# Optimization experiments

Hardware: AMD Instinct MI355X
Metric: run time of the kernel (lower is better)

## Reference

```python
import jax, jax.numpy as jnp
import numpy as np

EPS = 1e-5
G = 8    # groups
K = 3    # kernel_size


def bn(x, gamma, beta, mean, var):
    # inference-mode BatchNorm2d; x: (b,C,H,W), params: (C,)
    inv = gamma / jnp.sqrt(var + EPS)
    return x * inv[None, :, None, None] + (beta - mean * inv)[None, :, None, None]


def gconv1x1(x, w):
    # grouped 1x1 conv; x: (b, g*ci, H, W), w: (g, co, ci) -> (b, g*co, H, W)
    b, C, H, W = x.shape
    g, co, ci = w.shape
    xg = x.reshape(b, g, ci, H, W)
    y = jnp.einsum('bgihw,goi->bgohw', xg, w)
    return y.reshape(b, g * co, H, W)


def unfold3(x):
    # torch.nn.Unfold(k=3, stride=1, dilation=1, padding=1), reshaped to (b, C, 9, H, W)
    b, C, H, W = x.shape
    xp = jnp.pad(x, ((0, 0), (0, 0), (1, 1), (1, 1)))
    patches = [xp[:, :, i:i + H, j:j + W] for i in range(K) for j in range(K)]
    return jnp.stack(patches, axis=2)


def setup_inputs() -> dict:
    key = jax.random.key(0)
    ks = jax.random.split(key, 16)
    f = jax.random.normal
    u = jax.random.uniform
    return {
        'x':  f(ks[0], (2, 256, 128, 128), jnp.float32),
        'w1': f(ks[1], (8, 8, 32), jnp.float32) * 0.1,
        'b1': f(ks[2], (64,), jnp.float32) * 0.1,
        'g1': u(ks[3], (64,), jnp.float32, 0.5, 1.5),
        'be1': f(ks[4], (64,), jnp.float32) * 0.1,
        'm1': f(ks[5], (64,), jnp.float32) * 0.1,
        'v1': u(ks[6], (64,), jnp.float32, 0.5, 1.5),
        'w2': f(ks[7], (8, 10, 8), jnp.float32) * 0.1,
        'b2': f(ks[8], (80,), jnp.float32) * 0.1,
        'g2': u(ks[9], (80,), jnp.float32, 0.5, 1.5),
        'be2': f(ks[10], (80,), jnp.float32) * 0.1,
        'm2': f(ks[11], (80,), jnp.float32) * 0.1,
        'v2': u(ks[12], (80,), jnp.float32, 0.5, 1.5),
        'wv': f(ks[13], (8, 32, 32), jnp.float32) * 0.1,
    }


def reference(x, w1, b1, g1, be1, m1, v1, w2, b2, g2, be2, m2, v2, wv):
    b, C, H, W = x.shape
    # mask_conv: grouped 1x1 conv -> BN -> tanh -> grouped 1x1 conv -> BN
    t = jnp.tanh(bn(gconv1x1(x, w1) + b1[None, :, None, None], g1, be1, m1, v1))
    mn = bn(gconv1x1(t, w2) + b2[None, :, None, None], g2, be2, m2, v2)  # (b, G*(1+K*K), H, W)
    neighbor = mn[:, :G]          # (b, G, H, W)
    mask = mn[:, G:]              # (b, G*K*K, H, W)
    nb = unfold3(neighbor)        # (b, G, 9, H, W)
    logits = mask.reshape(b, G, K * K, H, W) + nb
    attn = jax.nn.softmax(logits, axis=2)               # (b, G, 9, H, W)
    # value path: grouped 1x1 conv (no bias) then unfold
    v = gconv1x1(x, wv)                                  # (b, C, H, W)
    vu = unfold3(v).reshape(b, G, C // G, K * K, H, W)   # (b, G, C/G, 9, H, W)
    out = jnp.einsum('bgkhw,bgckhw->bgchw', attn, vu)    # weighted sum over window
    return out.reshape(b, C, H, W)
```

## Files before the change

### kernel.cpp

```cpp
#include <hip/hip_runtime.h>
#include <hip/hip_bf16.h>

#define HW  16384
#define WD  128

#define TS   16
#define HS   18
#define HP   (HS * HS)
#define PRS  20
#define PLS  360

__device__ __forceinline__ unsigned short f2bf(float f) {
    unsigned int u = __builtin_bit_cast(unsigned int, f);
    u += 0x7FFFu + ((u >> 16) & 1u);
    return (unsigned short)(u >> 16);
}
__device__ __forceinline__ float bf2f(unsigned int s) {
    return __builtin_bit_cast(float, (s & 0xFFFFu) << 16);
}
__device__ __forceinline__ float ftanh(float v) {
    const float e = __expf(2.0f * v);
    return 1.0f - __fdividef(2.0f, e + 1.0f);
}

__global__ __launch_bounds__(256) void la_t(
    const float* __restrict__ x,
    const float* __restrict__ w1, const float* __restrict__ b1,
    const float* __restrict__ g1, const float* __restrict__ be1,
    const float* __restrict__ m1, const float* __restrict__ v1,
    const float* __restrict__ w2, const float* __restrict__ b2,
    const float* __restrict__ g2, const float* __restrict__ be2,
    const float* __restrict__ m2, const float* __restrict__ v2,
    unsigned short* __restrict__ t, float* __restrict__ nb)
{
    const int pix = blockIdx.x * blockDim.x + threadIdx.x;
    const int b   = blockIdx.y;
    const int p   = blockIdx.z;

    const float* xp = x + (size_t)(b * 256 + p * 32) * HW + pix;
    float xv[32];
#pragma unroll
    for (int c = 0; c < 32; ++c) xv[c] = xp[(size_t)c * HW];

    const float* w1p = w1 + p * 256;
    float tv[8];
#pragma unroll
    for (int o = 0; o < 8; ++o) {
        float a = 0.f;
#pragma unroll
        for (int ci = 0; ci < 32; ++ci) a = fmaf(xv[ci], w1p[o * 32 + ci], a);
        const int ch = p * 8 + o;
        const float inv = g1[ch] * rsqrtf(v1[ch] + 1e-5f);
        const float add = be1[ch] + (b1[ch] - m1[ch]) * inv;
        tv[o] = ftanh(fmaf(a, inv, add));
    }

    uint4 u;
    u.x = (unsigned)f2bf(tv[0]) | ((unsigned)f2bf(tv[1]) << 16);
    u.y = (unsigned)f2bf(tv[2]) | ((unsigned)f2bf(tv[3]) << 16);
    u.z = (unsigned)f2bf(tv[4]) | ((unsigned)f2bf(tv[5]) << 16);
    u.w = (unsigned)f2bf(tv[6]) | ((unsigned)f2bf(tv[7]) << 16);
    *(uint4*)(t + ((size_t)(b * 8 + p) * HW + pix) * 8) = u;

    if (p == 0) {
#pragma unroll
        for (int o = 0; o < 8; ++o) {
            float a = 0.f;
#pragma unroll
            for (int i = 0; i < 8; ++i) a = fmaf(tv[i], w2[o * 8 + i], a);
            const float inv = g2[o] * rsqrtf(v2[o] + 1e-5f);
            const float add = be2[o] + (b2[o] - m2[o]) * inv;
            nb[(size_t)(b * 8 + o) * HW + pix] = fmaf(a, inv, add);
        }
    }
}

__global__ __launch_bounds__(256, 4) void la_fused(
    const float* __restrict__ x,
    const float* __restrict__ w2, const float* __restrict__ b2,
    const float* __restrict__ g2, const float* __restrict__ be2,
    const float* __restrict__ m2, const float* __restrict__ v2,
    const float* __restrict__ wv,
    const unsigned short* __restrict__ t, const float* __restrict__ nb,
    float* __restrict__ out)
{
    __shared__ ushort4 xt[8 * PLS];
    __shared__ float   nbs[PLS];

    const int tid  = threadIdx.x;
    const int bg   = blockIdx.x;
    const int tile = blockIdx.y;
    const int b    = bg >> 3, g = bg & 7;
    const int ty0  = (tile >> 3) * TS;
    const int tx0  = (tile & 7) * TS;

    const float* xg  = x  + (size_t)(b * 256 + g * 32) * HW;
    const float* nbp = nb + (size_t)(b * 8 + g) * HW;

    for (int hp = tid; hp < HP; hp += 256) {
        const int hy = hp / HS, hx = hp - hy * HS;
        const int iy = ty0 + hy - 1, ix = tx0 + hx - 1;
        const int slot = hy * PRS + hx;
        if (((unsigned)iy < 128u) && ((unsigned)ix < 128u)) {
            const int po = iy * WD + ix;
            float xv[32];
#pragma unroll
            for (int c = 0; c < 32; ++c) xv[c] = xg[(size_t)c * HW + po];
            nbs[slot] = nbp[po];
#pragma unroll
            for (int c4 = 0; c4 < 8; ++c4)
                xt[c4 * PLS + slot] = make_ushort4(
                    f2bf(xv[c4 * 4 + 0]), f2bf(xv[c4 * 4 + 1]),
                    f2bf(xv[c4 * 4 + 2]), f2bf(xv[c4 * 4 + 3]));
        } else {
            const ushort4 z = make_ushort4(0, 0, 0, 0);
#pragma unroll
            for (int c4 = 0; c4 < 8; ++c4) xt[c4 * PLS + slot] = z;
            nbs[slot] = 0.f;
        }
    }
    __syncthreads();

    const int cy  = tid >> 4, cx = tid & 15;
    const int iy  = ty0 + cy, ix = tx0 + cx;
    const int pix = iy * WD + ix;

    const int mc0    = 8 + 9 * g;
    const int pa     = mc0 / 10;
    const int pb     = (mc0 + 8) / 10;
    const int ksplit = 10 - (mc0 - pa * 10);

    float tA[8], tB[8];
    {
        const uint4 ua = *(const uint4*)(t + ((size_t)(b * 8 + pa) * HW + pix) * 8);
        tA[0] = bf2f(ua.x); tA[1] = bf2f(ua.x >> 16);
        tA[2] = bf2f(ua.y); tA[3] = bf2f(ua.y >> 16);
        tA[4] = bf2f(ua.z); tA[5] = bf2f(ua.z >> 16);
        tA[6] = bf2f(ua.w); tA[7] = bf2f(ua.w >> 16);
    }
    if (pb != pa) {
        const uint4 ub = *(const uint4*)(t + ((size_t)(b * 8 + pb) * HW + pix) * 8);
        tB[0] = bf2f(ub.x); tB[1] = bf2f(ub.x >> 16);
        tB[2] = bf2f(ub.y); tB[3] = bf2f(ub.y >> 16);
        tB[4] = bf2f(ub.z); tB[5] = bf2f(ub.z >> 16);
        tB[6] = bf2f(ub.w); tB[7] = bf2f(ub.w >> 16);
    } else {
#pragma unroll
        for (int o = 0; o < 8; ++o) tB[o] = tA[o];
    }

    float lg[9];
    float mx = -1e30f;
#pragma unroll
    for (int k = 0; k < 9; ++k) {
        const int mc = mc0 + k;
        const int p  = (k < ksplit) ? pa : pb;
        const int o  = mc - p * 10;
        const float* w2p = w2 + p * 80 + o * 8;
        float a = 0.f;
#pragma unroll
        for (int i = 0; i < 8; ++i) {
            const float ti = (k < ksplit) ? tA[i] : tB[i];
            a = fmaf(ti, w2p[i], a);
        }
        const float inv = g2[mc] * rsqrtf(v2[mc] + 1e-5f);
        const float add = be2[mc] + (b2[mc] - m2[mc]) * inv;
        lg[k] = fmaf(a, inv, add) + nbs[(cy + k / 3) * PRS + (cx + k % 3)];
        mx = fmaxf(mx, lg[k]);
    }
    float ssum = 0.f;
#pragma unroll
    for (int k = 0; k < 9; ++k) { lg[k] = __expf(lg[k] - mx); ssum += lg[k]; }
    const float rs = 1.f / ssum;

    float s[32];
#pragma unroll
    for (int c = 0; c < 32; ++c) s[c] = 0.f;
#pragma unroll
    for (int k = 0; k < 9; ++k) {
        const int slot = (cy + k / 3) * PRS + (cx + k % 3);
        const float e = lg[k];
#pragma unroll
        for (int c4 = 0; c4 < 8; ++c4) {
            const ushort4 xv4 = xt[c4 * PLS + slot];
            s[c4 * 4 + 0] = fmaf(e, bf2f(xv4.x), s[c4 * 4 + 0]);
            s[c4 * 4 + 1] = fmaf(e, bf2f(xv4.y), s[c4 * 4 + 1]);
            s[c4 * 4 + 2] = fmaf(e, bf2f(xv4.z), s[c4 * 4 + 2]);
            s[c4 * 4 + 3] = fmaf(e, bf2f(xv4.w), s[c4 * 4 + 3]);
        }
    }

    const float* wvg = wv + g * 1024;
    float* og = out + (size_t)(b * 256 + g * 32) * HW + pix;
#pragma unroll 4
    for (int o = 0; o < 32; ++o) {
        const float* wp = wvg + o * 32;
        float a = 0.f;
#pragma unroll
        for (int ci = 0; ci < 32; ++ci) a = fmaf(s[ci], wp[ci], a);
        __builtin_nontemporal_store(a * rs, og + (size_t)o * HW);
    }
}

extern "C" void kernel_launch(void* const* d_in, const int* in_sizes, int n_in,
                              void* d_out, int out_size, void* d_ws, size_t ws_size,
                              hipStream_t stream)
{
    const float* x   = (const float*)d_in[0];
    const float* w1  = (const float*)d_in[1];
    const float* b1  = (const float*)d_in[2];
    const float* g1  = (const float*)d_in[3];
    const float* be1 = (const float*)d_in[4];
    const float* m1  = (const float*)d_in[5];
    const float* v1  = (const float*)d_in[6];
    const float* w2  = (const float*)d_in[7];
    const float* b2  = (const float*)d_in[8];
    const float* g2  = (const float*)d_in[9];
    const float* be2 = (const float*)d_in[10];
    const float* m2  = (const float*)d_in[11];
    const float* v2  = (const float*)d_in[12];
    const float* wv  = (const float*)d_in[13];

    float* out = (float*)d_out;
    unsigned short* t = (unsigned short*)d_ws;
    float* nb = (float*)(t + (size_t)2 * 8 * HW * 8);

    dim3 blk(256);
    dim3 gt(HW / 256, 2, 8);
    dim3 grd(16, 64);

    hipLaunchKernelGGL(la_t, gt, blk, 0, stream,
                       x, w1, b1, g1, be1, m1, v1, w2, b2, g2, be2, m2, v2,
                       t, nb);
    hipLaunchKernelGGL(la_fused, grd, blk, 0, stream,
                       x, w2, b2, g2, be2, m2, v2, wv, t, nb, out);
}
```

Baseline: 130.0 us.

## Fuse mask-conv stage into attention kernel, recomputing tanh features per tile

Merges the two launches into one kernel. Each block now recomputes the first grouped conv, BN and tanh for its own group over the halo tile and keeps the result in LDS. It also recomputes the neighbor logits from partition 0 per halo pixel, and the adjacent partition's features per center pixel. This removes the workspace round-trip for t/nb and one kernel launch. In exchange it adds redundant reads of x (partition 0 and the neighboring partition) and repeated conv1 compute, plus extra LDS use that may lower occupancy.

```diff
diff --git a/kernel.cpp b/kernel.cpp
--- a/kernel.cpp
+++ b/kernel.cpp
@@ -1,5 +1,4 @@
 #include <hip/hip_runtime.h>
-#include <hip/hip_bf16.h>
 
 #define HW  16384
 #define WD  128
@@ -23,7 +22,27 @@
     return 1.0f - __fdividef(2.0f, e + 1.0f);
 }
 
-__global__ __launch_bounds__(256) void la_t(
+__device__ __forceinline__ void conv1_bn_tanh(
+    const float xv[32], int p,
+    const float* __restrict__ w1, const float* __restrict__ g1,
+    const float* __restrict__ be1, const float* __restrict__ b1,
+    const float* __restrict__ m1, const float* __restrict__ v1,
+    float t[8])
+{
+    const float* w1g = w1 + p * 256;
+#pragma unroll
+    for (int o = 0; o < 8; ++o) {
+        float a = 0.f;
+#pragma unroll
+        for (int ci = 0; ci < 32; ++ci) a = fmaf(xv[ci], w1g[o * 32 + ci], a);
+        const int ch = p * 8 + o;
+        const float inv = g1[ch] * rsqrtf(v1[ch] + 1e-5f);
+        const float add = be1[ch] + (b1[ch] - m1[ch]) * inv;
+        t[o] = ftanh(fmaf(a, inv, add));
+    }
+}
+
+__global__ __launch_bounds__(256, 4) void la_all(
     const float* __restrict__ x,
     const float* __restrict__ w1, const float* __restrict__ b1,
     const float* __restrict__ g1, const float* __restrict__ be1,
@@ -31,60 +50,11 @@
     const float* __restrict__ w2, const float* __restrict__ b2,
     const float* __restrict__ g2, const float* __restrict__ be2,
     const float* __restrict__ m2, const float* __restrict__ v2,
-    unsigned short* __restrict__ t, float* __restrict__ nb)
-{
-    const int pix = blockIdx.x * blockDim.x + threadIdx.x;
-    const int b   = blockIdx.y;
-    const int p   = blockIdx.z;
-
-    const float* xp = x + (size_t)(b * 256 + p * 32) * HW + pix;
-    float xv[32];
-#pragma unroll
-    for (int c = 0; c < 32; ++c) xv[c] = xp[(size_t)c * HW];
-
-    const float* w1p = w1 + p * 256;
-    float tv[8];
-#pragma unroll
-    for (int o = 0; o < 8; ++o) {
-        float a = 0.f;
-#pragma unroll
-        for (int ci = 0; ci < 32; ++ci) a = fmaf(xv[ci], w1p[o * 32 + ci], a);
-        const int ch = p * 8 + o;
-        const float inv = g1[ch] * rsqrtf(v1[ch] + 1e-5f);
-        const float add = be1[ch] + (b1[ch] - m1[ch]) * inv;
-        tv[o] = ftanh(fmaf(a, inv, add));
-    }
-
-    uint4 u;
-    u.x = (unsigned)f2bf(tv[0]) | ((unsigned)f2bf(tv[1]) << 16);
-    u.y = (unsigned)f2bf(tv[2]) | ((unsigned)f2bf(tv[3]) << 16);
-    u.z = (unsigned)f2bf(tv[4]) | ((unsigned)f2bf(tv[5]) << 16);
-    u.w = (unsigned)f2bf(tv[6]) | ((unsigned)f2bf(tv[7]) << 16);
-    *(uint4*)(t + ((size_t)(b * 8 + p) * HW + pix) * 8) = u;
-
-    if (p == 0) {
-#pragma unroll
-        for (int o = 0; o < 8; ++o) {
-            float a = 0.f;
-#pragma unroll
-            for (int i = 0; i < 8; ++i) a = fmaf(tv[i], w2[o * 8 + i], a);
-            const float inv = g2[o] * rsqrtf(v2[o] + 1e-5f);
-            const float add = be2[o] + (b2[o] - m2[o]) * inv;
-            nb[(size_t)(b * 8 + o) * HW + pix] = fmaf(a, inv, add);
-        }
-    }
-}
-
-__global__ __launch_bounds__(256, 4) void la_fused(
-    const float* __restrict__ x,
-    const float* __restrict__ w2, const float* __restrict__ b2,
-    const float* __restrict__ g2, const float* __restrict__ be2,
-    const float* __restrict__ m2, const float* __restrict__ v2,
     const float* __restrict__ wv,
-    const unsigned short* __restrict__ t, const float* __restrict__ nb,
     float* __restrict__ out)
 {
     __shared__ ushort4 xt[8 * PLS];
+    __shared__ uint4   tls[PLS];
     __shared__ float   nbs[PLS];
 
     const int tid  = threadIdx.x;
@@ -94,8 +64,11 @@
     const int ty0  = (tile >> 3) * TS;
     const int tx0  = (tile & 7) * TS;
 
-    const float* xg  = x  + (size_t)(b * 256 + g * 32) * HW;
-    const float* nbp = nb + (size_t)(b * 8 + g) * HW;
+    const float* xb = x + (size_t)b * 256 * HW;
+    const float* xg = xb + (size_t)(g * 32) * HW;
+
+    const float inv2n = g2[g] * rsqrtf(v2[g] + 1e-5f);
+    const float add2n = be2[g] + (b2[g] - m2[g]) * inv2n;
 
     for (int hp = tid; hp < HP; hp += 256) {
         const int hy = hp / HS, hx = hp - hy * HS;
@@ -103,19 +76,46 @@
         const int slot = hy * PRS + hx;
         if (((unsigned)iy < 128u) && ((unsigned)ix < 128u)) {
             const int po = iy * WD + ix;
-            float xv[32];
-#pragma unroll
-            for (int c = 0; c < 32; ++c) xv[c] = xg[(size_t)c * HW + po];
-            nbs[slot] = nbp[po];
+            float xv[32], tg[8];
+            if (g == 0) {
+#pragma unroll
+                for (int c = 0; c < 32; ++c) xv[c] = xb[(size_t)c * HW + po];
+                conv1_bn_tanh(xv, 0, w1, g1, be1, b1, m1, v1, tg);
+                float an = 0.f;
+#pragma unroll
+                for (int i = 0; i < 8; ++i) an = fmaf(tg[i], w2[g * 8 + i], an);
+                nbs[slot] = fmaf(an, inv2n, add2n);
+            } else {
+                {
+                    float x0[32], t0[8];
+#pragma unroll
+                    for (int c = 0; c < 32; ++c) x0[c] = xb[(size_t)c * HW + po];
+                    conv1_bn_tanh(x0, 0, w1, g1, be1, b1, m1, v1, t0);
+                    float an = 0.f;
+#pragma unroll
+                    for (int i = 0; i < 8; ++i) an = fmaf(t0[i], w2[g * 8 + i], an);
+                    nbs[slot] = fmaf(an, inv2n, add2n);
+                }
+#pragma unroll
+                for (int c = 0; c < 32; ++c) xv[c] = xg[(size_t)c * HW + po];
+                conv1_bn_tanh(xv, g, w1, g1, be1, b1, m1, v1, tg);
+            }
 #pragma unroll
             for (int c4 = 0; c4 < 8; ++c4)
                 xt[c4 * PLS + slot] = make_ushort4(
                     f2bf(xv[c4 * 4 + 0]), f2bf(xv[c4 * 4 + 1]),
                     f2bf(xv[c4 * 4 + 2]), f2bf(xv[c4 * 4 + 3]));
+            uint4 tu;
+            tu.x = (unsigned)f2bf(tg[0]) | ((unsigned)f2bf(tg[1]) << 16);
+            tu.y = (unsigned)f2bf(tg[2]) | ((unsigned)f2bf(tg[3]) << 16);
+            tu.z = (unsigned)f2bf(tg[4]) | ((unsigned)f2bf(tg[5]) << 16);
+            tu.w = (unsigned)f2bf(tg[6]) | ((unsigned)f2bf(tg[7]) << 16);
+            tls[slot] = tu;
         } else {
             const ushort4 z = make_ushort4(0, 0, 0, 0);
 #pragma unroll
             for (int c4 = 0; c4 < 8; ++c4) xt[c4 * PLS + slot] = z;
+            tls[slot] = make_uint4(0u, 0u, 0u, 0u);
             nbs[slot] = 0.f;
         }
     }
@@ -132,18 +132,18 @@
 
     float tA[8], tB[8];
     {
-        const uint4 ua = *(const uint4*)(t + ((size_t)(b * 8 + pa) * HW + pix) * 8);
+        const uint4 ua = tls[(cy + 1) * PRS + (cx + 1)];
         tA[0] = bf2f(ua.x); tA[1] = bf2f(ua.x >> 16);
         tA[2] = bf2f(ua.y); tA[3] = bf2f(ua.y >> 16);
         tA[4] = bf2f(ua.z); tA[5] = bf2f(ua.z >> 16);
         tA[6] = bf2f(ua.w); tA[7] = bf2f(ua.w >> 16);
     }
     if (pb != pa) {
-        const uint4 ub = *(const uint4*)(t + ((size_t)(b * 8 + pb) * HW + pix) * 8);
-        tB[0] = bf2f(ub.x); tB[1] = bf2f(ub.x >> 16);
-        tB[2] = bf2f(ub.y); tB[3] = bf2f(ub.y >> 16);
-        tB[4] = bf2f(ub.z); tB[5] = bf2f(ub.z >> 16);
-        tB[6] = bf2f(ub.w); tB[7] = bf2f(ub.w >> 16);
+        float xv[32];
+        const float* xn = xb + (size_t)(pb * 32) * HW + pix;
+#pragma unroll
+        for (int c = 0; c < 32; ++c) xv[c] = xn[(size_t)c * HW];
+        conv1_bn_tanh(xv, pb, w1, g1, be1, b1, m1, v1, tB);
     } else {
 #pragma unroll
         for (int o = 0; o < 8; ++o) tB[o] = tA[o];
@@ -222,16 +222,12 @@
     const float* wv  = (const float*)d_in[13];
 
     float* out = (float*)d_out;
-    unsigned short* t = (unsigned short*)d_ws;
-    float* nb = (float*)(t + (size_t)2 * 8 * HW * 8);
+    (void)d_ws; (void)ws_size;
 
     dim3 blk(256);
-    dim3 gt(HW / 256, 2, 8);
     dim3 grd(16, 64);
 
-    hipLaunchKernelGGL(la_t, gt, blk, 0, stream,
+    hipLaunchKernelGGL(la_all, grd, blk, 0, stream,
                        x, w1, b1, g1, be1, m1, v1, w2, b2, g2, be2, m2, v2,
-                       t, nb);
-    hipLaunchKernelGGL(la_fused, grd, blk, 0, stream,
-                       x, w2, b2, g2, be2, m2, v2, wv, t, nb, out);
-}
+                       wv, out);
+}
```

Result: slower. 137.2 us (+5.6%).

## Move value projection and full mask conv into pre-pass kernel

Applied to the files above, without the earlier changes.

The first kernel now computes the value 1x1 grouped conv (stored as bf16) plus the full second mask conv (neighbor and mask logits) per pixel. The attention kernel then only gathers the bf16 value halo and the precomputed logits and writes the weighted sum directly. This removes the per-pixel 32x32 projection after aggregation and the t round-trip, but the pre-pass does more work and writes more intermediate data (bf16 v, plus the 72-channel mask in fp32). Because the projection now runs before the window sum, it is rounded to bf16 and reapplied to neighbor values, which changes the precision profile.

```diff
diff --git a/kernel.cpp b/kernel.cpp
--- a/kernel.cpp
+++ b/kernel.cpp
@@ -1,5 +1,4 @@
 #include <hip/hip_runtime.h>
-#include <hip/hip_bf16.h>
 
 #define HW  16384
 #define WD  128
@@ -23,7 +22,7 @@
     return 1.0f - __fdividef(2.0f, e + 1.0f);
 }
 
-__global__ __launch_bounds__(256) void la_t(
+__global__ __launch_bounds__(256) void la_pre(
     const float* __restrict__ x,
     const float* __restrict__ w1, const float* __restrict__ b1,
     const float* __restrict__ g1, const float* __restrict__ be1,
@@ -31,7 +30,8 @@
     const float* __restrict__ w2, const float* __restrict__ b2,
     const float* __restrict__ g2, const float* __restrict__ be2,
     const float* __restrict__ m2, const float* __restrict__ v2,
-    unsigned short* __restrict__ t, float* __restrict__ nb)
+    const float* __restrict__ wv,
+    uint4* __restrict__ v4, float* __restrict__ nb, float* __restrict__ mask)
 {
     const int pix = blockIdx.x * blockDim.x + threadIdx.x;
     const int b   = blockIdx.y;
@@ -42,49 +42,62 @@
 #pragma unroll
     for (int c = 0; c < 32; ++c) xv[c] = xp[(size_t)c * HW];
 
-    const float* w1p = w1 + p * 256;
+    const float* w1g = w1 + p * 256;
     float tv[8];
 #pragma unroll
     for (int o = 0; o < 8; ++o) {
         float a = 0.f;
 #pragma unroll
-        for (int ci = 0; ci < 32; ++ci) a = fmaf(xv[ci], w1p[o * 32 + ci], a);
+        for (int ci = 0; ci < 32; ++ci) a = fmaf(xv[ci], w1g[o * 32 + ci], a);
         const int ch = p * 8 + o;
         const float inv = g1[ch] * rsqrtf(v1[ch] + 1e-5f);
         const float add = be1[ch] + (b1[ch] - m1[ch]) * inv;
         tv[o] = ftanh(fmaf(a, inv, add));
     }
 
-    uint4 u;
-    u.x = (unsigned)f2bf(tv[0]) | ((unsigned)f2bf(tv[1]) << 16);
-    u.y = (unsigned)f2bf(tv[2]) | ((unsigned)f2bf(tv[3]) << 16);
-    u.z = (unsigned)f2bf(tv[4]) | ((unsigned)f2bf(tv[5]) << 16);
-    u.w = (unsigned)f2bf(tv[6]) | ((unsigned)f2bf(tv[7]) << 16);
-    *(uint4*)(t + ((size_t)(b * 8 + p) * HW + pix) * 8) = u;
-
-    if (p == 0) {
-#pragma unroll
-        for (int o = 0; o < 8; ++o) {
+#pragma unroll
+    for (int o = 0; o < 10; ++o) {
+        const int c = p * 10 + o;
+        float a = 0.f;
+#pragma unroll
+        for (int i = 0; i < 8; ++i) a = fmaf(tv[i], w2[p * 80 + o * 8 + i], a);
+        const float inv = g2[c] * rsqrtf(v2[c] + 1e-5f);
+        const float add = be2[c] + (b2[c] - m2[c]) * inv;
+        const float val = fmaf(a, inv, add);
+        if (c < 8) {
+            nb[(size_t)(b * 8 + c) * HW + pix] = val;
+        } else {
+            const int gk = c - 8, g = gk / 9, k = gk - 9 * g;
+            mask[((size_t)(b * 8 + g) * 9 + k) * HW + pix] = val;
+        }
+    }
+
+    const float* wvp = wv + p * 1024;
+#pragma unroll
+    for (int c8 = 0; c8 < 4; ++c8) {
+        float ov[8];
+#pragma unroll
+        for (int j = 0; j < 8; ++j) {
             float a = 0.f;
 #pragma unroll
-            for (int i = 0; i < 8; ++i) a = fmaf(tv[i], w2[o * 8 + i], a);
-            const float inv = g2[o] * rsqrtf(v2[o] + 1e-5f);
-            const float add = be2[o] + (b2[o] - m2[o]) * inv;
-            nb[(size_t)(b * 8 + o) * HW + pix] = fmaf(a, inv, add);
-        }
-    }
-}
-
-__global__ __launch_bounds__(256, 4) void la_fused(
-    const float* __restrict__ x,
-    const float* __restrict__ w2, const float* __restrict__ b2,
-    const float* __restrict__ g2, const float* __restrict__ be2,
-    const float* __restrict__ m2, const float* __restrict__ v2,
-    const float* __restrict__ wv,
-    const unsigned short* __restrict__ t, const float* __restrict__ nb,
-    float* __restrict__ out)
+            for (int ci = 0; ci < 32; ++ci)
+                a = fmaf(xv[ci], wvp[(c8 * 8 + j) * 32 + ci], a);
+            ov[j] = a;
+        }
+        uint4 u;
+        u.x = (unsigned)f2bf(ov[0]) | ((unsigned)f2bf(ov[1]) << 16);
+        u.y = (unsigned)f2bf(ov[2]) | ((unsigned)f2bf(ov[3]) << 16);
+        u.z = (unsigned)f2bf(ov[4]) | ((unsigned)f2bf(ov[5]) << 16);
+        u.w = (unsigned)f2bf(ov[6]) | ((unsigned)f2bf(ov[7]) << 16);
+        v4[((size_t)((b * 8 + p) * 4) + c8) * HW + pix] = u;
+    }
+}
+
+__global__ __launch_bounds__(256, 4) void la_attn(
+    const uint4* __restrict__ v4, const float* __restrict__ nb,
+    const float* __restrict__ mask, float* __restrict__ out)
 {
-    __shared__ ushort4 xt[8 * PLS];
+    __shared__ ushort4 vt[8 * PLS];
     __shared__ float   nbs[PLS];
 
     const int tid  = threadIdx.x;
@@ -94,78 +107,47 @@
     const int ty0  = (tile >> 3) * TS;
     const int tx0  = (tile & 7) * TS;
 
-    const float* xg  = x  + (size_t)(b * 256 + g * 32) * HW;
-    const float* nbp = nb + (size_t)(b * 8 + g) * HW;
-
-    for (int hp = tid; hp < HP; hp += 256) {
-        const int hy = hp / HS, hx = hp - hy * HS;
-        const int iy = ty0 + hy - 1, ix = tx0 + hx - 1;
-        const int slot = hy * PRS + hx;
-        if (((unsigned)iy < 128u) && ((unsigned)ix < 128u)) {
-            const int po = iy * WD + ix;
-            float xv[32];
-#pragma unroll
-            for (int c = 0; c < 32; ++c) xv[c] = xg[(size_t)c * HW + po];
-            nbs[slot] = nbp[po];
-#pragma unroll
-            for (int c4 = 0; c4 < 8; ++c4)
-                xt[c4 * PLS + slot] = make_ushort4(
-                    f2bf(xv[c4 * 4 + 0]), f2bf(xv[c4 * 4 + 1]),
-                    f2bf(xv[c4 * 4 + 2]), f2bf(xv[c4 * 4 + 3]));
-        } else {
-            const ushort4 z = make_ushort4(0, 0, 0, 0);
-#pragma unroll
-            for (int c4 = 0; c4 < 8; ++c4) xt[c4 * PLS + slot] = z;
-            nbs[slot] = 0.f;
-        }
-    }
-    __syncthreads();
-
     const int cy  = tid >> 4, cx = tid & 15;
     const int iy  = ty0 + cy, ix = tx0 + cx;
     const int pix = iy * WD + ix;
-
-    const int mc0    = 8 + 9 * g;
-    const int pa     = mc0 / 10;
-    const int pb     = (mc0 + 8) / 10;
-    const int ksplit = 10 - (mc0 - pa * 10);
-
-    float tA[8], tB[8];
-    {
-        const uint4 ua = *(const uint4*)(t + ((size_t)(b * 8 + pa) * HW + pix) * 8);
-        tA[0] = bf2f(ua.x); tA[1] = bf2f(ua.x >> 16);
-        tA[2] = bf2f(ua.y); tA[3] = bf2f(ua.y >> 16);
-        tA[4] = bf2f(ua.z); tA[5] = bf2f(ua.z >> 16);
-        tA[6] = bf2f(ua.w); tA[7] = bf2f(ua.w >> 16);
-    }
-    if (pb != pa) {
-        const uint4 ub = *(const uint4*)(t + ((size_t)(b * 8 + pb) * HW + pix) * 8);
-        tB[0] = bf2f(ub.x); tB[1] = bf2f(ub.x >> 16);
-        tB[2] = bf2f(ub.y); tB[3] = bf2f(ub.y >> 16);
-        tB[4] = bf2f(ub.z); tB[5] = bf2f(ub.z >> 16);
-        tB[6] = bf2f(ub.w); tB[7] = bf2f(ub.w >> 16);
-    } else {
-#pragma unroll
-        for (int o = 0; o < 8; ++o) tB[o] = tA[o];
-    }
+    const float* mp = mask + (size_t)(b * 8 + g) * 9 * HW + pix;
+    float mk[9];
+#pragma unroll
+    for (int k = 0; k < 9; ++k) mk[k] = mp[(size_t)k * HW];
+
+    const uint4* vg  = v4 + (size_t)((b * 8 + g) * 4) * HW;
+    const float* nbp = nb + (size_t)(b * 8 + g) * HW;
+    for (int hp = tid; hp < HP; hp += 256) {
+        const int hy = hp / HS, hx = hp - hy * HS;
+        const int hiy = ty0 + hy - 1, hix = tx0 + hx - 1;
+        const int slot = hy * PRS + hx;
+        if (((unsigned)hiy < 128u) && ((unsigned)hix < 128u)) {
+            const int po = hiy * WD + hix;
+            nbs[slot] = nbp[po];
+#pragma unroll
+            for (int c8 = 0; c8 < 4; ++c8) {
+                const uint4 u = vg[(size_t)c8 * HW + po];
+                vt[(2 * c8 + 0) * PLS + slot] = make_ushort4(
+                    (unsigned short)u.x, (unsigned short)(u.x >> 16),
+                    (unsigned short)u.y, (unsigned short)(u.y >> 16));
+                vt[(2 * c8 + 1) * PLS + slot] = make_ushort4(
+                    (unsigned short)u.z, (unsigned short)(u.z >> 16),
+                    (unsigned short)u.w, (unsigned short)(u.w >> 16));
+            }
+        } else {
+            const ushort4 z = make_ushort4(0, 0, 0, 0);
+#pragma unroll
+            for (int c4 = 0; c4 < 8; ++c4) vt[c4 * PLS + slot] = z;
+            nbs[slot] = 0.f;
+        }
+    }
+    __syncthreads();
 
     float lg[9];
     float mx = -1e30f;
 #pragma unroll
     for (int k = 0; k < 9; ++k) {
-        const int mc = mc0 + k;
-        const int p  = (k < ksplit) ? pa : pb;
-        const int o  = mc - p * 10;
-        const float* w2p = w2 + p * 80 + o * 8;
-        float a = 0.f;
-#pragma unroll
-        for (int i = 0; i < 8; ++i) {
-            const float ti = (k < ksplit) ? tA[i] : tB[i];
-            a = fmaf(ti, w2p[i], a);
-        }
-        const float inv = g2[mc] * rsqrtf(v2[mc] + 1e-5f);
-        const float add = be2[mc] + (b2[mc] - m2[mc]) * inv;
-        lg[k] = fmaf(a, inv, add) + nbs[(cy + k / 3) * PRS + (cx + k % 3)];
+        lg[k] = mk[k] + nbs[(cy + k / 3) * PRS + (cx + k % 3)];
         mx = fmaxf(mx, lg[k]);
     }
     float ssum = 0.f;
@@ -182,24 +164,18 @@
         const float e = lg[k];
 #pragma unroll
         for (int c4 = 0; c4 < 8; ++c4) {
-            const ushort4 xv4 = xt[c4 * PLS + slot];
-            s[c4 * 4 + 0] = fmaf(e, bf2f(xv4.x), s[c4 * 4 + 0]);
-            s[c4 * 4 + 1] = fmaf(e, bf2f(xv4.y), s[c4 * 4 + 1]);
-            s[c4 * 4 + 2] = fmaf(e, bf2f(xv4.z), s[c4 * 4 + 2]);
-            s[c4 * 4 + 3] = fmaf(e, bf2f(xv4.w), s[c4 * 4 + 3]);
-        }
-    }
-
-    const float* wvg = wv + g * 1024;
+            const ushort4 vv = vt[c4 * PLS + slot];
+            s[c4 * 4 + 0] = fmaf(e, bf2f(vv.x), s[c4 * 4 + 0]);
+            s[c4 * 4 + 1] = fmaf(e, bf2f(vv.y), s[c4 * 4 + 1]);
+            s[c4 * 4 + 2] = fmaf(e, bf2f(vv.z), s[c4 * 4 + 2]);
+            s[c4 * 4 + 3] = fmaf(e, bf2f(vv.w), s[c4 * 4 + 3]);
+        }
+    }
+
     float* og = out + (size_t)(b * 256 + g * 32) * HW + pix;
-#pragma unroll 4
-    for (int o = 0; o < 32; ++o) {
-        const float* wp = wvg + o * 32;
-        float a = 0.f;
-#pragma unroll
-        for (int ci = 0; ci < 32; ++ci) a = fmaf(s[ci], wp[ci], a);
-        __builtin_nontemporal_store(a * rs, og + (size_t)o * HW);
-    }
+#pragma unroll 8
+    for (int o = 0; o < 32; ++o)
+        __builtin_nontemporal_store(s[o] * rs, og + (size_t)o * HW);
 }
 
 extern "C" void kernel_launch(void* const* d_in, const int* in_sizes, int n_in,
@@ -222,16 +198,18 @@
     const float* wv  = (const float*)d_in[13];
 
     float* out = (float*)d_out;
-    unsigned short* t = (unsigned short*)d_ws;
-    float* nb = (float*)(t + (size_t)2 * 8 * HW * 8);
+
+    uint4* v4  = (uint4*)d_ws;
+    float* nbw = (float*)((char*)d_ws + (size_t)64 * HW * 16);
+    float* msk = nbw + (size_t)16 * HW;
 
     dim3 blk(256);
-    dim3 gt(HW / 256, 2, 8);
-    dim3 grd(16, 64);
-
-    hipLaunchKernelGGL(la_t, gt, blk, 0, stream,
+    dim3 gpre(HW / 256, 2, 8);
+    dim3 gatt(16, 64);
+
+    hipLaunchKernelGGL(la_pre, gpre, blk, 0, stream,
                        x, w1, b1, g1, be1, m1, v1, w2, b2, g2, be2, m2, v2,
-                       t, nb);
-    hipLaunchKernelGGL(la_fused, grd, blk, 0, stream,
-                       x, w2, b2, g2, be2, m2, v2, wv, t, nb, out);
-}
+                       wv, v4, nbw, msk);
+    hipLaunchKernelGGL(la_attn, gatt, blk, 0, stream,
+                       v4, nbw, msk, out);
+}
```

Measured after the change: 142.8 us. 1.1x slower.

## Split first conv across two half-blocks and compute neighbor logits in fused kernel

Applied to the files above, without the earlier changes.

The first kernel now splits each group's 8 output channels into two halves over twice as many blocks, storing t as two ushort4 planes. This removes the p==0 imbalance where one block slice also computed the neighbor map. The neighbor logits are now recomputed inside the fused kernel's halo load from t, so the nb buffer disappears. The cost is that every block of the first kernel rereads its 32 x channels twice, and the fused kernel does extra loads and FMAs per halo pixel.

```diff
diff --git a/kernel.cpp b/kernel.cpp
--- a/kernel.cpp
+++ b/kernel.cpp
@@ -1,5 +1,4 @@
 #include <hip/hip_runtime.h>
-#include <hip/hip_bf16.h>
 
 #define HW  16384
 #define WD  128
@@ -28,51 +27,34 @@
     const float* __restrict__ w1, const float* __restrict__ b1,
     const float* __restrict__ g1, const float* __restrict__ be1,
     const float* __restrict__ m1, const float* __restrict__ v1,
-    const float* __restrict__ w2, const float* __restrict__ b2,
-    const float* __restrict__ g2, const float* __restrict__ be2,
-    const float* __restrict__ m2, const float* __restrict__ v2,
-    unsigned short* __restrict__ t, float* __restrict__ nb)
+    ushort4* __restrict__ t4)
 {
     const int pix = blockIdx.x * blockDim.x + threadIdx.x;
     const int b   = blockIdx.y;
-    const int p   = blockIdx.z;
+    const int z   = blockIdx.z;
+    const int p   = z >> 1;
+    const int h   = z & 1;
 
     const float* xp = x + (size_t)(b * 256 + p * 32) * HW + pix;
     float xv[32];
 #pragma unroll
     for (int c = 0; c < 32; ++c) xv[c] = xp[(size_t)c * HW];
 
-    const float* w1p = w1 + p * 256;
-    float tv[8];
-#pragma unroll
-    for (int o = 0; o < 8; ++o) {
+    const float* w1g = w1 + p * 256 + h * 4 * 32;
+    float tv[4];
+#pragma unroll
+    for (int o = 0; o < 4; ++o) {
         float a = 0.f;
 #pragma unroll
-        for (int ci = 0; ci < 32; ++ci) a = fmaf(xv[ci], w1p[o * 32 + ci], a);
-        const int ch = p * 8 + o;
+        for (int ci = 0; ci < 32; ++ci) a = fmaf(xv[ci], w1g[o * 32 + ci], a);
+        const int ch = p * 8 + h * 4 + o;
         const float inv = g1[ch] * rsqrtf(v1[ch] + 1e-5f);
         const float add = be1[ch] + (b1[ch] - m1[ch]) * inv;
         tv[o] = ftanh(fmaf(a, inv, add));
     }
 
-    uint4 u;
-    u.x = (unsigned)f2bf(tv[0]) | ((unsigned)f2bf(tv[1]) << 16);
-    u.y = (unsigned)f2bf(tv[2]) | ((unsigned)f2bf(tv[3]) << 16);
-    u.z = (unsigned)f2bf(tv[4]) | ((unsigned)f2bf(tv[5]) << 16);
-    u.w = (unsigned)f2bf(tv[6]) | ((unsigned)f2bf(tv[7]) << 16);
-    *(uint4*)(t + ((size_t)(b * 8 + p) * HW + pix) * 8) = u;
-
-    if (p == 0) {
-#pragma unroll
-        for (int o = 0; o < 8; ++o) {
-            float a = 0.f;
-#pragma unroll
-            for (int i = 0; i < 8; ++i) a = fmaf(tv[i], w2[o * 8 + i], a);
-            const float inv = g2[o] * rsqrtf(v2[o] + 1e-5f);
-            const float add = be2[o] + (b2[o] - m2[o]) * inv;
-            nb[(size_t)(b * 8 + o) * HW + pix] = fmaf(a, inv, add);
-        }
-    }
+    t4[((size_t)((b * 8 + p) * 2 + h)) * HW + pix] =
+        make_ushort4(f2bf(tv[0]), f2bf(tv[1]), f2bf(tv[2]), f2bf(tv[3]));
 }
 
 __global__ __launch_bounds__(256, 4) void la_fused(
@@ -81,7 +63,7 @@
     const float* __restrict__ g2, const float* __restrict__ be2,
     const float* __restrict__ m2, const float* __restrict__ v2,
     const float* __restrict__ wv,
-    const unsigned short* __restrict__ t, const float* __restrict__ nb,
+    const ushort4* __restrict__ t4,
     float* __restrict__ out)
 {
     __shared__ ushort4 xt[8 * PLS];
@@ -94,8 +76,11 @@
     const int ty0  = (tile >> 3) * TS;
     const int tx0  = (tile & 7) * TS;
 
-    const float* xg  = x  + (size_t)(b * 256 + g * 32) * HW;
-    const float* nbp = nb + (size_t)(b * 8 + g) * HW;
+    const float*   xg  = x  + (size_t)(b * 256 + g * 32) * HW;
+    const ushort4* t0  = t4 + (size_t)(b * 16) * HW;
+
+    const float inv2n = g2[g] * rsqrtf(v2[g] + 1e-5f);
+    const float add2n = be2[g] + (b2[g] - m2[g]) * inv2n;
 
     for (int hp = tid; hp < HP; hp += 256) {
         const int hy = hp / HS, hx = hp - hy * HS;
@@ -106,7 +91,18 @@
             float xv[32];
 #pragma unroll
             for (int c = 0; c < 32; ++c) xv[c] = xg[(size_t)c * HW + po];
-            nbs[slot] = nbp[po];
+            const ushort4 ta = t0[po];
+            const ushort4 tb = t0[(size_t)HW + po];
+            float an = 0.f;
+            an = fmaf(bf2f(ta.x), w2[g * 8 + 0], an);
+            an = fmaf(bf2f(ta.y), w2[g * 8 + 1], an);
+            an = fmaf(bf2f(ta.z), w2[g * 8 + 2], an);
+            an = fmaf(bf2f(ta.w), w2[g * 8 + 3], an);
+            an = fmaf(bf2f(tb.x), w2[g * 8 + 4], an);
+            an = fmaf(bf2f(tb.y), w2[g * 8 + 5], an);
+            an = fmaf(bf2f(tb.z), w2[g * 8 + 6], an);
+            an = fmaf(bf2f(tb.w), w2[g * 8 + 7], an);
+            nbs[slot] = fmaf(an, inv2n, add2n);
 #pragma unroll
             for (int c4 = 0; c4 < 8; ++c4)
                 xt[c4 * PLS + slot] = make_ushort4(
@@ -132,18 +128,20 @@
 
     float tA[8], tB[8];
     {
-        const uint4 ua = *(const uint4*)(t + ((size_t)(b * 8 + pa) * HW + pix) * 8);
-        tA[0] = bf2f(ua.x); tA[1] = bf2f(ua.x >> 16);
-        tA[2] = bf2f(ua.y); tA[3] = bf2f(ua.y >> 16);
-        tA[4] = bf2f(ua.z); tA[5] = bf2f(ua.z >> 16);
-        tA[6] = bf2f(ua.w); tA[7] = bf2f(ua.w >> 16);
+        const ushort4 lo = t4[((size_t)((b * 8 + pa) * 2 + 0)) * HW + pix];
+        const ushort4 hi = t4[((size_t)((b * 8 + pa) * 2 + 1)) * HW + pix];
+        tA[0] = bf2f(lo.x); tA[1] = bf2f(lo.y);
+        tA[2] = bf2f(lo.z); tA[3] = bf2f(lo.w);
+        tA[4] = bf2f(hi.x); tA[5] = bf2f(hi.y);
+        tA[6] = bf2f(hi.z); tA[7] = bf2f(hi.w);
     }
     if (pb != pa) {
-        const uint4 ub = *(const uint4*)(t + ((size_t)(b * 8 + pb) * HW + pix) * 8);
-        tB[0] = bf2f(ub.x); tB[1] = bf2f(ub.x >> 16);
-        tB[2] = bf2f(ub.y); tB[3] = bf2f(ub.y >> 16);
-        tB[4] = bf2f(ub.z); tB[5] = bf2f(ub.z >> 16);
-        tB[6] = bf2f(ub.w); tB[7] = bf2f(ub.w >> 16);
+        const ushort4 lo = t4[((size_t)((b * 8 + pb) * 2 + 0)) * HW + pix];
+        const ushort4 hi = t4[((size_t)((b * 8 + pb) * 2 + 1)) * HW + pix];
+        tB[0] = bf2f(lo.x); tB[1] = bf2f(lo.y);
+        tB[2] = bf2f(lo.z); tB[3] = bf2f(lo.w);
+        tB[4] = bf2f(hi.x); tB[5] = bf2f(hi.y);
+        tB[6] = bf2f(hi.z); tB[7] = bf2f(hi.w);
     } else {
 #pragma unroll
         for (int o = 0; o < 8; ++o) tB[o] = tA[o];
@@ -222,16 +220,14 @@
     const float* wv  = (const float*)d_in[13];
 
     float* out = (float*)d_out;
-    unsigned short* t = (unsigned short*)d_ws;
-    float* nb = (float*)(t + (size_t)2 * 8 * HW * 8);
+    ushort4* t4 = (ushort4*)d_ws;
 
     dim3 blk(256);
-    dim3 gt(HW / 256, 2, 8);
+    dim3 gt(HW / 256, 2, 16);
     dim3 grd(16, 64);
 
     hipLaunchKernelGGL(la_t, gt, blk, 0, stream,
-                       x, w1, b1, g1, be1, m1, v1, w2, b2, g2, be2, m2, v2,
-                       t, nb);
+                       x, w1, b1, g1, be1, m1, v1, t4);
     hipLaunchKernelGGL(la_fused, grd, blk, 0, stream,
-                       x, w2, b2, g2, be2, m2, v2, wv, t, nb, out);
-}
+                       x, w2, b2, g2, be2, m2, v2, wv, t4, out);
+}
```

Result: faster. 126.8 us (-2.5%).
